# Kernel tuning notes

Hardware: AMD Instinct MI355X
Metric: run time of the kernel (lower is better)

The kernel has to match this reference:

```python
import jax, jax.numpy as jnp
import numpy as np

NUM_TREES = 32
TREE_DEPTH = 6
INPUT_DIM = 256
SHRINKAGE = 0.1
PHI_NUMEL = 1
N_INTERNAL = (1 << TREE_DEPTH) - 1  # 63, heap-ordered (level by level)
N_LEAVES = 1 << TREE_DEPTH          # 64


def setup_inputs() -> dict:
    key = jax.random.key(0)
    kx, kw, kb, kp = jax.random.split(key, 4)
    x = jax.random.normal(kx, (16384, INPUT_DIM), dtype=jnp.float32)
    # All internal-node Linear(input_dim,1) weights, batched: [T, N, F], biases [T, N]
    lim = 1.0 / np.sqrt(INPUT_DIM)  # torch nn.Linear default uniform init scale
    W = jax.random.uniform(kw, (NUM_TREES, N_INTERNAL, INPUT_DIM), minval=-lim, maxval=lim, dtype=jnp.float32)
    b = jax.random.uniform(kb, (NUM_TREES, N_INTERNAL), minval=-lim, maxval=lim, dtype=jnp.float32)
    # Leaf values phi: [T, L, P] (original: randn per leaf)
    phi = jax.random.normal(kp, (NUM_TREES, N_LEAVES, PHI_NUMEL), dtype=jnp.float32)
    return {"x": x, "W": W, "b": b, "phi": phi}


def reference(x, W, b, phi):
    B = x.shape[0]
    T, N, F = W.shape
    # One batched GEMM for every internal node of every tree, then sigmoid.
    # probs[b, t, n] = sigmoid(x[b] . W[t, n] + b[t, n]); heap order: node n at
    # level d occupies slots [2^d - 1, 2^(d+1) - 2], children of slot i are 2i, 2i+1.
    probs = jax.nn.sigmoid(jnp.einsum('bf,tnf->btn', x, W) + b)  # [B, T, N]
    # Path probabilities down the tree: left child gets (1 - p), right gets p
    # (matches calculate_probabilities: left <- pp*(1-prob), right <- pp*prob).
    mu = jnp.ones((B, T, 1), dtype=probs.dtype)
    offset = 0
    depth = int(np.log2(N + 1))
    for d in range(depth):
        n = 1 << d
        p = probs[:, :, offset:offset + n]                      # [B, T, n]
        mu = jnp.stack([mu * (1.0 - p), mu * p], axis=-1)       # [B, T, n, 2]
        mu = mu.reshape(B, T, 2 * n)
        offset += n
    # mu: [B, T, L] leaf path probabilities. Per-tree pred = sum_l mu_l * phi_l;
    # GBM output = shrinkage * sum over trees.
    pred = SHRINKAGE * jnp.einsum('btl,tlp->bp', mu, phi)       # [B, P]
    return pred
```

## Files before the change

### kernel.cpp

```cpp
#include <hip/hip_runtime.h>
#include <cmath>

typedef unsigned short u16;
typedef __bf16 bf16x8 __attribute__((ext_vector_type(8)));
typedef float f32x4 __attribute__((ext_vector_type(4)));
typedef unsigned short u16x4 __attribute__((ext_vector_type(4)));

#define BATCH 16384
#define NTREE 32
#define NINT 63
#define NLEAF 64
#define FDIM 256
#define MT 128
#define TPB 2
#define BK 64
#define KSTEPS 4

typedef __attribute__((address_space(3))) void lvoid;
typedef __attribute__((address_space(1))) const void gvoid;
__device__ __forceinline__ void gload16(const void* g, void* l) {
    __builtin_amdgcn_global_load_lds((gvoid*)g, (lvoid*)l, 16, 0, 0);
}

__device__ __forceinline__ u16 f2bf(float f) {
    unsigned int x = __float_as_uint(f);
    x += 0x7fffu + ((x >> 16) & 1u);
    return (u16)(x >> 16);
}

__device__ __forceinline__ int slot2node(int slot) {
    int lg = (slot >> 2) & 3;
    int v = ((slot >> 4) << 2) | (slot & 3);
    if (v == 0)  return (lg & 1) ? (1 + (lg >> 1)) : 0;
    if (v == 1)  return 3 + lg;
    if (v < 4)   return 7 + 2 * lg + (v - 2);
    if (v < 8)   return 15 + 4 * lg + (v - 4);
    return 31 + 8 * lg + (v - 8);
}

__global__ void convert_kernel(const float* __restrict__ x, const float* __restrict__ W,
                               const float* __restrict__ b,
                               u16* __restrict__ xb, u16* __restrict__ Wb,
                               float* __restrict__ bperm) {
    int idx = blockIdx.x * blockDim.x + threadIdx.x;
    int stride = gridDim.x * blockDim.x;
    const int NXQ = BATCH * FDIM / 4;
    for (int i = idx; i < NXQ; i += stride) {
        float4 v = ((const float4*)x)[i];
        u16x4 o = { f2bf(v.x), f2bf(v.y), f2bf(v.z), f2bf(v.w) };
        ((u16x4*)xb)[i] = o;
    }
    const int NWQ = NTREE * NLEAF * FDIM / 4;
    for (int i = idx; i < NWQ; i += stride) {
        int t = i / (NLEAF * FDIM / 4);
        int r = i % (NLEAF * FDIM / 4);
        int slot = r / (FDIM / 4);
        int kq = r % (FDIM / 4);
        int node = slot2node(slot);
        float4 v = ((const float4*)(W + ((size_t)t * NINT + node) * FDIM))[kq];
        u16x4 o = { f2bf(v.x), f2bf(v.y), f2bf(v.z), f2bf(v.w) };
        ((u16x4*)Wb)[i] = o;
    }
    if (idx < NTREE * NLEAF)
        bperm[idx] = b[(idx >> 6) * NINT + slot2node(idx & 63)];
}

__global__ __launch_bounds__(256, 3) void softgbm_main(
    const u16* __restrict__ xb, const u16* __restrict__ Wb,
    const float* __restrict__ bperm, const float* __restrict__ phig,
    float* __restrict__ partial) {
    __shared__ u16 Ash[MT * BK];
    __shared__ u16 Bsh[MT * BK];

    const int tid = threadIdx.x;
    const int lane = tid & 63, wv = tid >> 6;
    const int t0 = blockIdx.y * TPB;
    const int m0 = blockIdx.x * MT;
    const int th = wv & 1, rh = wv >> 1;
    const int frow = lane & 15, lg = lane >> 4, f7 = frow & 7;

    const int row0 = wv * 32 + (lane >> 3);
    const int cc = (lane & 7) ^ ((lane >> 3) & 7);
    const u16* ag = Wb + (size_t)(t0 * NLEAF + row0) * FDIM + cc * 8;
    const u16* bg2 = xb + (size_t)(m0 + row0) * FDIM + cc * 8;

    const int abase = (th * 64 + frow) * 128;
    const int bbase = (rh * 64 + frow) * 128;
    const int koff0 = (lg ^ f7) * 16;
    const int koff1 = ((4 + lg) ^ f7) * 16;

    float bl[16];
    #pragma unroll
    for (int v2 = 0; v2 < 16; ++v2)
        bl[v2] = bperm[(t0 + th) * 64 + (v2 >> 2) * 16 + lg * 4 + (v2 & 3)];
    float pha[8], phd[8];
    #pragma unroll
    for (int i = 0; i < 8; ++i) {
        float2 p2 = *(const float2*)&phig[(size_t)(t0 + th) * NLEAF + lg * 16 + 2 * i];
        pha[i] = p2.x; phd[i] = p2.y - p2.x;
    }

    f32x4 acc[4][4] = {};
    #pragma unroll
    for (int st = 0; st < KSTEPS; ++st) {
        if (st) __syncthreads();
        #pragma unroll
        for (int j = 0; j < 4; ++j) {
            gload16(ag + st * BK + j * 8 * FDIM, &Ash[(wv * 256 + j * 64) * 8]);
            gload16(bg2 + st * BK + j * 8 * FDIM, &Bsh[(wv * 256 + j * 64) * 8]);
        }
        __syncthreads();
        #pragma unroll
        for (int ks = 0; ks < 2; ++ks) {
            const int ko = ks ? koff1 : koff0;
            bf16x8 af[4], bf_[4];
            #pragma unroll
            for (int ar = 0; ar < 4; ++ar)
                af[ar] = *(const bf16x8*)((const char*)Ash + abase + ar * 2048 + ko);
            #pragma unroll
            for (int bc = 0; bc < 4; ++bc)
                bf_[bc] = *(const bf16x8*)((const char*)Bsh + bbase + bc * 2048 + ko);
            #pragma unroll
            for (int ar = 0; ar < 4; ++ar)
                #pragma unroll
                for (int bc = 0; bc < 4; ++bc)
                    acc[ar][bc] = __builtin_amdgcn_mfma_f32_16x16x32_bf16(af[ar], bf_[bc], acc[ar][bc], 0, 0, 0);
        }
    }

    float tot[4];
    #pragma unroll
    for (int bc = 0; bc < 4; ++bc) {
        float pv[16];
        #pragma unroll
        for (int v2 = 0; v2 < 16; ++v2) {
            float z = acc[v2 >> 2][bc][v2 & 3] + bl[v2];
            pv[v2] = __builtin_amdgcn_rcpf(1.f + __expf(-z));
        }
        float o = __shfl_xor(pv[0], 16);
        float proot = (lg & 1) ? o : pv[0];
        float pd1   = (lg & 1) ? pv[0] : o;
        float mb = ((lg >> 1) ? proot : 1.f - proot) * ((lg & 1) ? pd1 : 1.f - pd1);
        float m3[2], m4[4], m5[8];
        { float t1 = mb * pv[1]; m3[1] = t1; m3[0] = mb - t1; }
        #pragma unroll
        for (int i = 0; i < 2; ++i) { float t1 = m3[i] * pv[2 + i]; m4[2*i+1] = t1; m4[2*i] = m3[i] - t1; }
        #pragma unroll
        for (int i = 0; i < 4; ++i) { float t1 = m4[i] * pv[4 + i]; m5[2*i+1] = t1; m5[2*i] = m4[i] - t1; }
        float s = 0.f;
        #pragma unroll
        for (int i = 0; i < 8; ++i) s += m5[i] * (pha[i] + pv[8 + i] * phd[i]);
        s += __shfl_xor(s, 16);
        s += __shfl_xor(s, 32);
        tot[bc] = s;
    }
    float vout = (lg & 2) ? ((lg & 1) ? tot[3] : tot[2])
                          : ((lg & 1) ? tot[1] : tot[0]);
    partial[(size_t)(t0 + th) * BATCH + m0 + rh * 64 + lane] = vout;
}

__global__ void reduce_kernel(const float* __restrict__ partial, float* __restrict__ out) {
    int i = blockIdx.x * 256 + threadIdx.x;
    float s = 0.f;
    #pragma unroll
    for (int t = 0; t < NTREE; ++t) s += partial[(size_t)t * BATCH + i];
    out[i] = 0.1f * s;
}

extern "C" void kernel_launch(void* const* d_in, const int* in_sizes, int n_in,
                              void* d_out, int out_size, void* d_ws, size_t ws_size,
                              hipStream_t stream) {
    const float* x   = (const float*)d_in[0];
    const float* W   = (const float*)d_in[1];
    const float* b   = (const float*)d_in[2];
    const float* phi = (const float*)d_in[3];
    float* out = (float*)d_out;

    u16* xb = (u16*)d_ws;
    u16* Wb = xb + (size_t)BATCH * FDIM;
    float* partial = (float*)(Wb + (size_t)NTREE * NLEAF * FDIM);
    float* bperm = partial + (size_t)NTREE * BATCH;

    convert_kernel<<<2048, 256, 0, stream>>>(x, W, b, xb, Wb, bperm);
    softgbm_main<<<dim3(BATCH / MT, NTREE / TPB), 256, 0, stream>>>(xb, Wb, bperm, phi, partial);
    reduce_kernel<<<BATCH / 256, 256, 0, stream>>>(partial, out);
}
```

Baseline: 37.60 us.

## Keep full X tile resident in LDS and loop over 16 trees per block

Each block now loads its whole 128x256 bf16 input tile into LDS once and iterates over 16 trees in pairs. Tree weights stream through a double-buffered LDS tile so the next W chunk loads while the current one is consumed. Partial sums are accumulated in registers across trees, cutting the partial buffer and the reduce pass from 32 slices to 4. The trade-off is a 2-row grid of 256 blocks with about 128KB of LDS per block, so occupancy drops to about one block per CU, and the trees within a block are processed serially.

```diff
diff --git a/kernel.cpp b/kernel.cpp
--- a/kernel.cpp
+++ b/kernel.cpp
@@ -12,9 +12,8 @@
 #define NLEAF 64
 #define FDIM 256
 #define MT 128
-#define TPB 2
-#define BK 64
-#define KSTEPS 4
+#define THALF 16
+#define NSTEP 16
 
 typedef __attribute__((address_space(3))) void lvoid;
 typedef __attribute__((address_space(1))) const void gvoid;
@@ -65,105 +64,139 @@
         bperm[idx] = b[(idx >> 6) * NINT + slot2node(idx & 63)];
 }
 
-__global__ __launch_bounds__(256, 3) void softgbm_main(
+__global__ __launch_bounds__(256) void softgbm_main(
     const u16* __restrict__ xb, const u16* __restrict__ Wb,
     const float* __restrict__ bperm, const float* __restrict__ phig,
     float* __restrict__ partial) {
-    __shared__ u16 Ash[MT * BK];
-    __shared__ u16 Bsh[MT * BK];
+    __shared__ u16 X[MT * FDIM];
+    __shared__ u16 Wt[2][MT * 128];
 
     const int tid = threadIdx.x;
     const int lane = tid & 63, wv = tid >> 6;
-    const int t0 = blockIdx.y * TPB;
+    const int rg = wv >> 1, tp = wv & 1;
+    const int ttop = blockIdx.y * THALF;
     const int m0 = blockIdx.x * MT;
-    const int th = wv & 1, rh = wv >> 1;
     const int frow = lane & 15, lg = lane >> 4, f7 = frow & 7;
 
-    const int row0 = wv * 32 + (lane >> 3);
-    const int cc = (lane & 7) ^ ((lane >> 3) & 7);
-    const u16* ag = Wb + (size_t)(t0 * NLEAF + row0) * FDIM + cc * 8;
-    const u16* bg2 = xb + (size_t)(m0 + row0) * FDIM + cc * 8;
-
-    const int abase = (th * 64 + frow) * 128;
-    const int bbase = (rh * 64 + frow) * 128;
-    const int koff0 = (lg ^ f7) * 16;
-    const int koff1 = ((4 + lg) ^ f7) * 16;
-
-    float bl[16];
-    #pragma unroll
-    for (int v2 = 0; v2 < 16; ++v2)
-        bl[v2] = bperm[(t0 + th) * 64 + (v2 >> 2) * 16 + lg * 4 + (v2 & 3)];
-    float pha[8], phd[8];
-    #pragma unroll
-    for (int i = 0; i < 8; ++i) {
-        float2 p2 = *(const float2*)&phig[(size_t)(t0 + th) * NLEAF + lg * 16 + 2 * i];
-        pha[i] = p2.x; phd[i] = p2.y - p2.x;
-    }
-
-    f32x4 acc[4][4] = {};
-    #pragma unroll
-    for (int st = 0; st < KSTEPS; ++st) {
-        if (st) __syncthreads();
-        #pragma unroll
-        for (int j = 0; j < 4; ++j) {
-            gload16(ag + st * BK + j * 8 * FDIM, &Ash[(wv * 256 + j * 64) * 8]);
-            gload16(bg2 + st * BK + j * 8 * FDIM, &Bsh[(wv * 256 + j * 64) * 8]);
-        }
-        __syncthreads();
-        #pragma unroll
-        for (int ks = 0; ks < 2; ++ks) {
-            const int ko = ks ? koff1 : koff0;
-            bf16x8 af[4], bf_[4];
-            #pragma unroll
-            for (int ar = 0; ar < 4; ++ar)
-                af[ar] = *(const bf16x8*)((const char*)Ash + abase + ar * 2048 + ko);
-            #pragma unroll
-            for (int bc = 0; bc < 4; ++bc)
-                bf_[bc] = *(const bf16x8*)((const char*)Bsh + bbase + bc * 2048 + ko);
-            #pragma unroll
-            for (int ar = 0; ar < 4; ++ar)
+    #pragma unroll
+    for (int i = 0; i < 16; ++i) {
+        int cl = i * 256 + wv * 64 + lane;
+        int row = cl >> 5, pcc = cl & 31;
+        int cc = (pcc & 24) | ((pcc & 7) ^ (row & 7));
+        gload16(xb + (size_t)(m0 + row) * FDIM + cc * 8, &X[cl * 8]);
+    }
+    int wrowcc[8], wdst[8];
+    #pragma unroll
+    for (int j = 0; j < 8; ++j) {
+        int cl = j * 256 + wv * 64 + lane;
+        int row = cl >> 4, pcc = cl & 15;
+        int cc = (pcc & 8) | ((pcc & 7) ^ (row & 7));
+        wrowcc[j] = row * FDIM + cc * 8;
+        wdst[j] = cl * 8;
+    }
+    const u16* wpairbase = Wb + (size_t)ttop * NLEAF * FDIM;
+    #pragma unroll
+    for (int j = 0; j < 8; ++j)
+        gload16(wpairbase + wrowcc[j], &Wt[0][wdst[j]]);
+
+    int Abase[4], Bbase[4], aoff[4], xoff[2][4];
+    #pragma unroll
+    for (int ar = 0; ar < 4; ++ar) Abase[ar] = (tp * 64 + ar * 16 + frow) * 256;
+    #pragma unroll
+    for (int bc = 0; bc < 4; ++bc) Bbase[bc] = (rg * 64 + bc * 16 + frow) * 512;
+    #pragma unroll
+    for (int ks = 0; ks < 4; ++ks) {
+        int c = ks * 4 + lg;
+        aoff[ks] = ((c & 8) | ((c & 7) ^ f7)) * 16;
+        #pragma unroll
+        for (int kh = 0; kh < 2; ++kh) {
+            int cx = kh * 16 + ks * 4 + lg;
+            xoff[kh][ks] = ((cx & 24) | ((cx & 7) ^ f7)) * 16;
+        }
+    }
+
+    float rsum = 0.f;
+    for (int pair = 0; pair < 8; ++pair) {
+        const int t = ttop + pair * 2 + tp;
+        float bl[16];
+        #pragma unroll
+        for (int v2 = 0; v2 < 16; ++v2)
+            bl[v2] = bperm[t * 64 + (v2 >> 2) * 16 + lg * 4 + (v2 & 3)];
+        float pha[8], phd[8];
+        #pragma unroll
+        for (int i = 0; i < 8; ++i) {
+            float2 p2 = *(const float2*)&phig[(size_t)t * NLEAF + lg * 16 + 2 * i];
+            pha[i] = p2.x; phd[i] = p2.y - p2.x;
+        }
+
+        f32x4 acc[4][4] = {};
+        #pragma unroll
+        for (int kh = 0; kh < 2; ++kh) {
+            const int step = pair * 2 + kh;
+            __syncthreads();
+            if (step + 1 < NSTEP) {
+                int np = (step + 1) >> 1, nk = (step + 1) & 1;
+                const u16* ws = wpairbase + (size_t)np * 128 * FDIM + nk * 128;
+                u16* wd = Wt[(step + 1) & 1];
+                #pragma unroll
+                for (int j = 0; j < 8; ++j)
+                    gload16(ws + wrowcc[j], &wd[wdst[j]]);
+            }
+            const char* Wc = (const char*)Wt[step & 1];
+            const char* Xc = (const char*)X;
+            #pragma unroll
+            for (int ks = 0; ks < 4; ++ks) {
+                bf16x8 af[4], bf_[4];
+                #pragma unroll
+                for (int ar = 0; ar < 4; ++ar)
+                    af[ar] = *(const bf16x8*)(Wc + Abase[ar] + aoff[ks]);
                 #pragma unroll
                 for (int bc = 0; bc < 4; ++bc)
-                    acc[ar][bc] = __builtin_amdgcn_mfma_f32_16x16x32_bf16(af[ar], bf_[bc], acc[ar][bc], 0, 0, 0);
-        }
-    }
-
-    float tot[4];
-    #pragma unroll
-    for (int bc = 0; bc < 4; ++bc) {
-        float pv[16];
-        #pragma unroll
-        for (int v2 = 0; v2 < 16; ++v2) {
-            float z = acc[v2 >> 2][bc][v2 & 3] + bl[v2];
-            pv[v2] = __builtin_amdgcn_rcpf(1.f + __expf(-z));
-        }
-        float o = __shfl_xor(pv[0], 16);
-        float proot = (lg & 1) ? o : pv[0];
-        float pd1   = (lg & 1) ? pv[0] : o;
-        float mb = ((lg >> 1) ? proot : 1.f - proot) * ((lg & 1) ? pd1 : 1.f - pd1);
-        float m3[2], m4[4], m5[8];
-        { float t1 = mb * pv[1]; m3[1] = t1; m3[0] = mb - t1; }
-        #pragma unroll
-        for (int i = 0; i < 2; ++i) { float t1 = m3[i] * pv[2 + i]; m4[2*i+1] = t1; m4[2*i] = m3[i] - t1; }
-        #pragma unroll
-        for (int i = 0; i < 4; ++i) { float t1 = m4[i] * pv[4 + i]; m5[2*i+1] = t1; m5[2*i] = m4[i] - t1; }
-        float s = 0.f;
-        #pragma unroll
-        for (int i = 0; i < 8; ++i) s += m5[i] * (pha[i] + pv[8 + i] * phd[i]);
-        s += __shfl_xor(s, 16);
-        s += __shfl_xor(s, 32);
-        tot[bc] = s;
-    }
-    float vout = (lg & 2) ? ((lg & 1) ? tot[3] : tot[2])
-                          : ((lg & 1) ? tot[1] : tot[0]);
-    partial[(size_t)(t0 + th) * BATCH + m0 + rh * 64 + lane] = vout;
+                    bf_[bc] = *(const bf16x8*)(Xc + Bbase[bc] + xoff[kh][ks]);
+                #pragma unroll
+                for (int ar = 0; ar < 4; ++ar)
+                    #pragma unroll
+                    for (int bc = 0; bc < 4; ++bc)
+                        acc[ar][bc] = __builtin_amdgcn_mfma_f32_16x16x32_bf16(af[ar], bf_[bc], acc[ar][bc], 0, 0, 0);
+            }
+        }
+
+        float tot[4];
+        #pragma unroll
+        for (int bc = 0; bc < 4; ++bc) {
+            float pv[16];
+            #pragma unroll
+            for (int v2 = 0; v2 < 16; ++v2) {
+                float z = acc[v2 >> 2][bc][v2 & 3] + bl[v2];
+                pv[v2] = __builtin_amdgcn_rcpf(1.f + __expf(-z));
+            }
+            float o = __shfl_xor(pv[0], 16);
+            float proot = (lg & 1) ? o : pv[0];
+            float pd1   = (lg & 1) ? pv[0] : o;
+            float mb = ((lg >> 1) ? proot : 1.f - proot) * ((lg & 1) ? pd1 : 1.f - pd1);
+            float m3[2], m4[4], m5[8];
+            { float t1 = mb * pv[1]; m3[1] = t1; m3[0] = mb - t1; }
+            #pragma unroll
+            for (int i = 0; i < 2; ++i) { float t1 = m3[i] * pv[2 + i]; m4[2*i+1] = t1; m4[2*i] = m3[i] - t1; }
+            #pragma unroll
+            for (int i = 0; i < 4; ++i) { float t1 = m4[i] * pv[4 + i]; m5[2*i+1] = t1; m5[2*i] = m4[i] - t1; }
+            float s = 0.f;
+            #pragma unroll
+            for (int i = 0; i < 8; ++i) s += m5[i] * (pha[i] + pv[8 + i] * phd[i]);
+            s += __shfl_xor(s, 16);
+            s += __shfl_xor(s, 32);
+            tot[bc] = s;
+        }
+        float vout = (lg & 2) ? ((lg & 1) ? tot[3] : tot[2])
+                              : ((lg & 1) ? tot[1] : tot[0]);
+        rsum += vout;
+    }
+    partial[(size_t)(blockIdx.y * 2 + tp) * BATCH + m0 + rg * 64 + lane] = rsum;
 }
 
 __global__ void reduce_kernel(const float* __restrict__ partial, float* __restrict__ out) {
     int i = blockIdx.x * 256 + threadIdx.x;
-    float s = 0.f;
-    #pragma unroll
-    for (int t = 0; t < NTREE; ++t) s += partial[(size_t)t * BATCH + i];
+    float s = partial[i] + partial[BATCH + i] + partial[2 * BATCH + i] + partial[3 * BATCH + i];
     out[i] = 0.1f * s;
 }
 
@@ -179,9 +212,9 @@
     u16* xb = (u16*)d_ws;
     u16* Wb = xb + (size_t)BATCH * FDIM;
     float* partial = (float*)(Wb + (size_t)NTREE * NLEAF * FDIM);
-    float* bperm = partial + (size_t)NTREE * BATCH;
+    float* bperm = partial + (size_t)4 * BATCH;
 
     convert_kernel<<<2048, 256, 0, stream>>>(x, W, b, xb, Wb, bperm);
-    softgbm_main<<<dim3(BATCH / MT, NTREE / TPB), 256, 0, stream>>>(xb, Wb, bperm, phi, partial);
+    softgbm_main<<<dim3(BATCH / MT, 2), 256, 0, stream>>>(xb, Wb, bperm, phi, partial);
     reduce_kernel<<<BATCH / 256, 256, 0, stream>>>(partial, out);
 }
```

After: 45.07 us. 19.9% more time.

## Keep per-tree W fragments in registers and stream x directly from global

Applied to the files above, without the earlier changes.

Each wave now owns one tree and holds that tree's full 64x256 bf16 weight fragment in registers. It loops over eight 32-row strips of x, loading x straight from global memory with a one-step register prefetch. This drops LDS staging and block-wide barriers, and grid blocks now cover 256 rows by 4 trees. The cost is heavy register pressure (128 VGPRs for W alone, with occupancy hint lowered to 2), uncoalesced global reads of x, and each x row being re-read once per wave/tree instead of shared across waves through LDS.

```diff
diff --git a/kernel.cpp b/kernel.cpp
--- a/kernel.cpp
+++ b/kernel.cpp
@@ -11,16 +11,6 @@
 #define NINT 63
 #define NLEAF 64
 #define FDIM 256
-#define MT 128
-#define TPB 2
-#define BK 64
-#define KSTEPS 4
-
-typedef __attribute__((address_space(3))) void lvoid;
-typedef __attribute__((address_space(1))) const void gvoid;
-__device__ __forceinline__ void gload16(const void* g, void* l) {
-    __builtin_amdgcn_global_load_lds((gvoid*)g, (lvoid*)l, 16, 0, 0);
-}
 
 __device__ __forceinline__ u16 f2bf(float f) {
     unsigned int x = __float_as_uint(f);
@@ -65,98 +55,92 @@
         bperm[idx] = b[(idx >> 6) * NINT + slot2node(idx & 63)];
 }
 
-__global__ __launch_bounds__(256, 3) void softgbm_main(
+__global__ __launch_bounds__(256, 2) void softgbm_main(
     const u16* __restrict__ xb, const u16* __restrict__ Wb,
     const float* __restrict__ bperm, const float* __restrict__ phig,
     float* __restrict__ partial) {
-    __shared__ u16 Ash[MT * BK];
-    __shared__ u16 Bsh[MT * BK];
+    const int tid = threadIdx.x;
+    const int lane = tid & 63, tp = tid >> 6;
+    const int t = blockIdx.y * 4 + tp;
+    const int m0 = blockIdx.x * 256;
+    const int frow = lane & 15, lg = lane >> 4;
 
-    const int tid = threadIdx.x;
-    const int lane = tid & 63, wv = tid >> 6;
-    const int t0 = blockIdx.y * TPB;
-    const int m0 = blockIdx.x * MT;
-    const int th = wv & 1, rh = wv >> 1;
-    const int frow = lane & 15, lg = lane >> 4, f7 = frow & 7;
-
-    const int row0 = wv * 32 + (lane >> 3);
-    const int cc = (lane & 7) ^ ((lane >> 3) & 7);
-    const u16* ag = Wb + (size_t)(t0 * NLEAF + row0) * FDIM + cc * 8;
-    const u16* bg2 = xb + (size_t)(m0 + row0) * FDIM + cc * 8;
-
-    const int abase = (th * 64 + frow) * 128;
-    const int bbase = (rh * 64 + frow) * 128;
-    const int koff0 = (lg ^ f7) * 16;
-    const int koff1 = ((4 + lg) ^ f7) * 16;
+    const u16* wbase = Wb + (size_t)t * NLEAF * FDIM + frow * FDIM + lg * 8;
+    bf16x8 wfr[4][8];
+    #pragma unroll
+    for (int ar = 0; ar < 4; ++ar)
+        #pragma unroll
+        for (int ks = 0; ks < 8; ++ks)
+            wfr[ar][ks] = *(const bf16x8*)(wbase + ar * 16 * FDIM + ks * 32);
 
     float bl[16];
     #pragma unroll
     for (int v2 = 0; v2 < 16; ++v2)
-        bl[v2] = bperm[(t0 + th) * 64 + (v2 >> 2) * 16 + lg * 4 + (v2 & 3)];
+        bl[v2] = bperm[t * 64 + (v2 >> 2) * 16 + lg * 4 + (v2 & 3)];
     float pha[8], phd[8];
     #pragma unroll
     for (int i = 0; i < 8; ++i) {
-        float2 p2 = *(const float2*)&phig[(size_t)(t0 + th) * NLEAF + lg * 16 + 2 * i];
+        float2 p2 = *(const float2*)&phig[(size_t)t * NLEAF + lg * 16 + 2 * i];
         pha[i] = p2.x; phd[i] = p2.y - p2.x;
     }
 
-    f32x4 acc[4][4] = {};
-    #pragma unroll
-    for (int st = 0; st < KSTEPS; ++st) {
-        if (st) __syncthreads();
+    const u16* xrow = xb + (size_t)(m0 + frow) * FDIM + lg * 8;
+
+    for (int strip = 0; strip < 8; ++strip) {
+        const u16* xs = xrow + (size_t)strip * 32 * FDIM;
+        bf16x8 xf[2][2];
         #pragma unroll
-        for (int j = 0; j < 4; ++j) {
-            gload16(ag + st * BK + j * 8 * FDIM, &Ash[(wv * 256 + j * 64) * 8]);
-            gload16(bg2 + st * BK + j * 8 * FDIM, &Bsh[(wv * 256 + j * 64) * 8]);
-        }
-        __syncthreads();
+        for (int k0 = 0; k0 < 2; ++k0)
+            #pragma unroll
+            for (int bc = 0; bc < 2; ++bc)
+                xf[k0][bc] = *(const bf16x8*)(xs + bc * 16 * FDIM + k0 * 32);
+
+        f32x4 acc[4][2] = {};
         #pragma unroll
-        for (int ks = 0; ks < 2; ++ks) {
-            const int ko = ks ? koff1 : koff0;
-            bf16x8 af[4], bf_[4];
-            #pragma unroll
-            for (int ar = 0; ar < 4; ++ar)
-                af[ar] = *(const bf16x8*)((const char*)Ash + abase + ar * 2048 + ko);
-            #pragma unroll
-            for (int bc = 0; bc < 4; ++bc)
-                bf_[bc] = *(const bf16x8*)((const char*)Bsh + bbase + bc * 2048 + ko);
+        for (int ks = 0; ks < 8; ++ks) {
+            bf16x8 xn[2];
+            if (ks < 6) {
+                #pragma unroll
+                for (int bc = 0; bc < 2; ++bc)
+                    xn[bc] = *(const bf16x8*)(xs + bc * 16 * FDIM + (ks + 2) * 32);
+            }
             #pragma unroll
             for (int ar = 0; ar < 4; ++ar)
                 #pragma unroll
-                for (int bc = 0; bc < 4; ++bc)
-                    acc[ar][bc] = __builtin_amdgcn_mfma_f32_16x16x32_bf16(af[ar], bf_[bc], acc[ar][bc], 0, 0, 0);
+                for (int bc = 0; bc < 2; ++bc)
+                    acc[ar][bc] = __builtin_amdgcn_mfma_f32_16x16x32_bf16(wfr[ar][ks], xf[ks & 1][bc], acc[ar][bc], 0, 0, 0);
+            if (ks < 6) { xf[ks & 1][0] = xn[0]; xf[ks & 1][1] = xn[1]; }
         }
+
+        float tot[2];
+        #pragma unroll
+        for (int bc = 0; bc < 2; ++bc) {
+            float pv[16];
+            #pragma unroll
+            for (int v2 = 0; v2 < 16; ++v2) {
+                float z = acc[v2 >> 2][bc][v2 & 3] + bl[v2];
+                pv[v2] = __builtin_amdgcn_rcpf(1.f + __expf(-z));
+            }
+            float o = __shfl_xor(pv[0], 16);
+            float proot = (lg & 1) ? o : pv[0];
+            float pd1   = (lg & 1) ? pv[0] : o;
+            float mb = ((lg >> 1) ? proot : 1.f - proot) * ((lg & 1) ? pd1 : 1.f - pd1);
+            float m3[2], m4[4], m5[8];
+            { float t1 = mb * pv[1]; m3[1] = t1; m3[0] = mb - t1; }
+            #pragma unroll
+            for (int i = 0; i < 2; ++i) { float t1 = m3[i] * pv[2 + i]; m4[2*i+1] = t1; m4[2*i] = m3[i] - t1; }
+            #pragma unroll
+            for (int i = 0; i < 4; ++i) { float t1 = m4[i] * pv[4 + i]; m5[2*i+1] = t1; m5[2*i] = m4[i] - t1; }
+            float s = 0.f;
+            #pragma unroll
+            for (int i = 0; i < 8; ++i) s += m5[i] * (pha[i] + pv[8 + i] * phd[i]);
+            s += __shfl_xor(s, 16);
+            s += __shfl_xor(s, 32);
+            tot[bc] = s;
+        }
+        if (lg < 2)
+            partial[(size_t)t * BATCH + m0 + strip * 32 + lg * 16 + frow] = lg ? tot[1] : tot[0];
     }
-
-    float tot[4];
-    #pragma unroll
-    for (int bc = 0; bc < 4; ++bc) {
-        float pv[16];
-        #pragma unroll
-        for (int v2 = 0; v2 < 16; ++v2) {
-            float z = acc[v2 >> 2][bc][v2 & 3] + bl[v2];
-            pv[v2] = __builtin_amdgcn_rcpf(1.f + __expf(-z));
-        }
-        float o = __shfl_xor(pv[0], 16);
-        float proot = (lg & 1) ? o : pv[0];
-        float pd1   = (lg & 1) ? pv[0] : o;
-        float mb = ((lg >> 1) ? proot : 1.f - proot) * ((lg & 1) ? pd1 : 1.f - pd1);
-        float m3[2], m4[4], m5[8];
-        { float t1 = mb * pv[1]; m3[1] = t1; m3[0] = mb - t1; }
-        #pragma unroll
-        for (int i = 0; i < 2; ++i) { float t1 = m3[i] * pv[2 + i]; m4[2*i+1] = t1; m4[2*i] = m3[i] - t1; }
-        #pragma unroll
-        for (int i = 0; i < 4; ++i) { float t1 = m4[i] * pv[4 + i]; m5[2*i+1] = t1; m5[2*i] = m4[i] - t1; }
-        float s = 0.f;
-        #pragma unroll
-        for (int i = 0; i < 8; ++i) s += m5[i] * (pha[i] + pv[8 + i] * phd[i]);
-        s += __shfl_xor(s, 16);
-        s += __shfl_xor(s, 32);
-        tot[bc] = s;
-    }
-    float vout = (lg & 2) ? ((lg & 1) ? tot[3] : tot[2])
-                          : ((lg & 1) ? tot[1] : tot[0]);
-    partial[(size_t)(t0 + th) * BATCH + m0 + rh * 64 + lane] = vout;
 }
 
 __global__ void reduce_kernel(const float* __restrict__ partial, float* __restrict__ out) {
@@ -182,6 +166,6 @@
     float* bperm = partial + (size_t)NTREE * BATCH;
 
     convert_kernel<<<2048, 256, 0, stream>>>(x, W, b, xb, Wb, bperm);
-    softgbm_main<<<dim3(BATCH / MT, NTREE / TPB), 256, 0, stream>>>(xb, Wb, bperm, phi, partial);
+    softgbm_main<<<dim3(BATCH / 256, NTREE / 4), 256, 0, stream>>>(xb, Wb, bperm, phi, partial);
     reduce_kernel<<<BATCH / 256, 256, 0, stream>>>(partial, out);
 }
```

Measured after the change: 50.69 us. +34.8%, slower.

## Keep full X tile in LDS and per-tree W fragments in registers

Applied to the files above, without the earlier changes.

The main kernel now loads the whole 128x256 bf16 X tile into LDS once, with a swizzle, and has each wave own one tree. Each wave holds all of that tree's W fragments in registers, read straight from global memory. The 128 rows are processed in two halves, and the bias is folded into the accumulator init. This removes the per-K-step synchronisation and the W staging through LDS, and quadruples X reuse across trees per block (4 trees instead of 2). The cost is much higher register pressure (32 bf16x8 W fragments plus 64 accumulators), so launch bounds drop to 2 blocks per SM, and LDS grows to 64KB.

```diff
diff --git a/kernel.cpp b/kernel.cpp
--- a/kernel.cpp
+++ b/kernel.cpp
@@ -12,9 +12,6 @@
 #define NLEAF 64
 #define FDIM 256
 #define MT 128
-#define TPB 2
-#define BK 64
-#define KSTEPS 4
 
 typedef __attribute__((address_space(3))) void lvoid;
 typedef __attribute__((address_space(1))) const void gvoid;
@@ -65,98 +62,108 @@
         bperm[idx] = b[(idx >> 6) * NINT + slot2node(idx & 63)];
 }
 
-__global__ __launch_bounds__(256, 3) void softgbm_main(
+__global__ __launch_bounds__(256, 2) void softgbm_main(
     const u16* __restrict__ xb, const u16* __restrict__ Wb,
     const float* __restrict__ bperm, const float* __restrict__ phig,
     float* __restrict__ partial) {
-    __shared__ u16 Ash[MT * BK];
-    __shared__ u16 Bsh[MT * BK];
+    __shared__ u16 X[MT * FDIM];
 
     const int tid = threadIdx.x;
     const int lane = tid & 63, wv = tid >> 6;
-    const int t0 = blockIdx.y * TPB;
+    const int t = blockIdx.y * 4 + wv;
     const int m0 = blockIdx.x * MT;
-    const int th = wv & 1, rh = wv >> 1;
     const int frow = lane & 15, lg = lane >> 4, f7 = frow & 7;
 
-    const int row0 = wv * 32 + (lane >> 3);
-    const int cc = (lane & 7) ^ ((lane >> 3) & 7);
-    const u16* ag = Wb + (size_t)(t0 * NLEAF + row0) * FDIM + cc * 8;
-    const u16* bg2 = xb + (size_t)(m0 + row0) * FDIM + cc * 8;
-
-    const int abase = (th * 64 + frow) * 128;
-    const int bbase = (rh * 64 + frow) * 128;
-    const int koff0 = (lg ^ f7) * 16;
-    const int koff1 = ((4 + lg) ^ f7) * 16;
-
-    float bl[16];
     #pragma unroll
-    for (int v2 = 0; v2 < 16; ++v2)
-        bl[v2] = bperm[(t0 + th) * 64 + (v2 >> 2) * 16 + lg * 4 + (v2 & 3)];
-    float pha[8], phd[8];
-    #pragma unroll
-    for (int i = 0; i < 8; ++i) {
-        float2 p2 = *(const float2*)&phig[(size_t)(t0 + th) * NLEAF + lg * 16 + 2 * i];
-        pha[i] = p2.x; phd[i] = p2.y - p2.x;
+    for (int i = 0; i < 16; ++i) {
+        int cl = i * 256 + tid;
+        int row = cl >> 5, pcc = cl & 31;
+        int cc = (pcc & 24) | ((pcc & 7) ^ (row & 7));
+        gload16(xb + (size_t)(m0 + row) * FDIM + cc * 8, &X[cl * 8]);
     }
 
-    f32x4 acc[4][4] = {};
+    const u16* wbase = Wb + (size_t)t * NLEAF * FDIM + frow * FDIM + lg * 8;
+    bf16x8 wfr[4][8];
     #pragma unroll
-    for (int st = 0; st < KSTEPS; ++st) {
-        if (st) __syncthreads();
+    for (int ar = 0; ar < 4; ++ar)
         #pragma unroll
-        for (int j = 0; j < 4; ++j) {
-            gload16(ag + st * BK + j * 8 * FDIM, &Ash[(wv * 256 + j * 64) * 8]);
-            gload16(bg2 + st * BK + j * 8 * FDIM, &Bsh[(wv * 256 + j * 64) * 8]);
-        }
-        __syncthreads();
+        for (int ks = 0; ks < 8; ++ks)
+            wfr[ar][ks] = *(const bf16x8*)(wbase + ar * 16 * FDIM + ks * 32);
+
+    int xoff[8];
+    #pragma unroll
+    for (int ks = 0; ks < 8; ++ks) {
+        int cx = ks * 4 + lg;
+        xoff[ks] = ((cx & 24) | ((cx & 7) ^ f7)) * 16;
+    }
+
+    __syncthreads();
+
+    #pragma unroll
+    for (int half = 0; half < 2; ++half) {
+        f32x4 acc[4][4];
         #pragma unroll
-        for (int ks = 0; ks < 2; ++ks) {
-            const int ko = ks ? koff1 : koff0;
-            bf16x8 af[4], bf_[4];
+        for (int ar = 0; ar < 4; ++ar)
             #pragma unroll
-            for (int ar = 0; ar < 4; ++ar)
-                af[ar] = *(const bf16x8*)((const char*)Ash + abase + ar * 2048 + ko);
+            for (int j = 0; j < 4; ++j) {
+                float bv = bperm[t * 64 + ar * 16 + lg * 4 + j];
+                #pragma unroll
+                for (int bc = 0; bc < 4; ++bc) acc[ar][bc][j] = bv;
+            }
+
+        const char* Xc = (const char*)X;
+        int rbase[4];
+        #pragma unroll
+        for (int bc = 0; bc < 4; ++bc)
+            rbase[bc] = (half * 64 + bc * 16 + frow) * 512;
+
+        #pragma unroll
+        for (int ks = 0; ks < 8; ++ks) {
+            bf16x8 xf[4];
             #pragma unroll
             for (int bc = 0; bc < 4; ++bc)
-                bf_[bc] = *(const bf16x8*)((const char*)Bsh + bbase + bc * 2048 + ko);
+                xf[bc] = *(const bf16x8*)(Xc + rbase[bc] + xoff[ks]);
             #pragma unroll
             for (int ar = 0; ar < 4; ++ar)
                 #pragma unroll
                 for (int bc = 0; bc < 4; ++bc)
-                    acc[ar][bc] = __builtin_amdgcn_mfma_f32_16x16x32_bf16(af[ar], bf_[bc], acc[ar][bc], 0, 0, 0);
+                    acc[ar][bc] = __builtin_amdgcn_mfma_f32_16x16x32_bf16(wfr[ar][ks], xf[bc], acc[ar][bc], 0, 0, 0);
         }
+
+        float pha[8], phd[8];
+        #pragma unroll
+        for (int i = 0; i < 8; ++i) {
+            float2 p2 = *(const float2*)&phig[(size_t)t * NLEAF + lg * 16 + 2 * i];
+            pha[i] = p2.x; phd[i] = p2.y - p2.x;
+        }
+        float tot[4];
+        #pragma unroll
+        for (int bc = 0; bc < 4; ++bc) {
+            float pv[16];
+            #pragma unroll
+            for (int v2 = 0; v2 < 16; ++v2)
+                pv[v2] = __builtin_amdgcn_rcpf(1.f + __expf(-acc[v2 >> 2][bc][v2 & 3]));
+            float o = __shfl_xor(pv[0], 16);
+            float proot = (lg & 1) ? o : pv[0];
+            float pd1   = (lg & 1) ? pv[0] : o;
+            float mb = ((lg >> 1) ? proot : 1.f - proot) * ((lg & 1) ? pd1 : 1.f - pd1);
+            float m3[2], m4[4], m5[8];
+            { float t1 = mb * pv[1]; m3[1] = t1; m3[0] = mb - t1; }
+            #pragma unroll
+            for (int i = 0; i < 2; ++i) { float t1 = m3[i] * pv[2 + i]; m4[2*i+1] = t1; m4[2*i] = m3[i] - t1; }
+            #pragma unroll
+            for (int i = 0; i < 4; ++i) { float t1 = m4[i] * pv[4 + i]; m5[2*i+1] = t1; m5[2*i] = m4[i] - t1; }
+            float s = 0.f;
+            #pragma unroll
+            for (int i = 0; i < 8; ++i) s += m5[i] * (pha[i] + pv[8 + i] * phd[i]);
+            s += __shfl_xor(s, 16);
+            s += __shfl_xor(s, 32);
+            tot[bc] = s;
+        }
+        float vout = (lg & 2) ? ((lg & 1) ? tot[3] : tot[2])
+                              : ((lg & 1) ? tot[1] : tot[0]);
+        partial[(size_t)t * BATCH + m0 + half * 64 + lane] = vout;
     }
-
-    float tot[4];
-    #pragma unroll
-    for (int bc = 0; bc < 4; ++bc) {
-        float pv[16];
-        #pragma unroll
-        for (int v2 = 0; v2 < 16; ++v2) {
-            float z = acc[v2 >> 2][bc][v2 & 3] + bl[v2];
-            pv[v2] = __builtin_amdgcn_rcpf(1.f + __expf(-z));
-        }
-        float o = __shfl_xor(pv[0], 16);
-        float proot = (lg & 1) ? o : pv[0];
-        float pd1   = (lg & 1) ? pv[0] : o;
-        float mb = ((lg >> 1) ? proot : 1.f - proot) * ((lg & 1) ? pd1 : 1.f - pd1);
-        float m3[2], m4[4], m5[8];
-        { float t1 = mb * pv[1]; m3[1] = t1; m3[0] = mb - t1; }
-        #pragma unroll
-        for (int i = 0; i < 2; ++i) { float t1 = m3[i] * pv[2 + i]; m4[2*i+1] = t1; m4[2*i] = m3[i] - t1; }
-        #pragma unroll
-        for (int i = 0; i < 4; ++i) { float t1 = m4[i] * pv[4 + i]; m5[2*i+1] = t1; m5[2*i] = m4[i] - t1; }
-        float s = 0.f;
-        #pragma unroll
-        for (int i = 0; i < 8; ++i) s += m5[i] * (pha[i] + pv[8 + i] * phd[i]);
-        s += __shfl_xor(s, 16);
-        s += __shfl_xor(s, 32);
-        tot[bc] = s;
-    }
-    float vout = (lg & 2) ? ((lg & 1) ? tot[3] : tot[2])
-                          : ((lg & 1) ? tot[1] : tot[0]);
-    partial[(size_t)(t0 + th) * BATCH + m0 + rh * 64 + lane] = vout;
 }
 
 __global__ void reduce_kernel(const float* __restrict__ partial, float* __restrict__ out) {
@@ -182,6 +189,6 @@
     float* bperm = partial + (size_t)NTREE * BATCH;
 
     convert_kernel<<<2048, 256, 0, stream>>>(x, W, b, xb, Wb, bperm);
-    softgbm_main<<<dim3(BATCH / MT, NTREE / TPB), 256, 0, stream>>>(xb, Wb, bperm, phi, partial);
+    softgbm_main<<<dim3(BATCH / MT, NTREE / 4), 256, 0, stream>>>(xb, Wb, bperm, phi, partial);
     reduce_kernel<<<BATCH / 256, 256, 0, stream>>>(partial, out);
 }
```

Result: slower. 43.74 us (+16.3%).
